# Performance work log

Measured on AMD Instinct MI355X. Metric: run time of the kernel, lower is better.

Reference implementation:

```python
import jax, jax.numpy as jnp
import numpy as np

T, D_MODEL, D_FF, N_EXPERTS, TOPK = 4096, 2048, 8192, 8, 2


def setup_inputs() -> dict:
    key = jax.random.key(0)
    k1, k2, k3, k4 = jax.random.split(key, 4)
    x = jax.random.normal(k1, (T, D_MODEL), dtype=jnp.float32)
    gating_output = jax.random.normal(k2, (T, N_EXPERTS), dtype=jnp.float32)
    # gate_proj and up_proj concatenated along output dim: [E, 2*d_ff, d_model]
    gate_up_proj = jax.random.normal(k3, (N_EXPERTS, 2 * D_FF, D_MODEL), dtype=jnp.float32) * 0.02
    # down_proj: [E, d_model, d_ff]
    down_proj = jax.random.normal(k4, (N_EXPERTS, D_MODEL, D_FF), dtype=jnp.float32) * 0.02
    return {"x": x, "gating_output": gating_output, "gate_up_proj": gate_up_proj,
            "down_proj": down_proj, "topk": TOPK}


def reference(x, gating_output, gate_up_proj, down_proj, topk):
    n_experts = gate_up_proj.shape[0]
    d_ff = down_proj.shape[2]
    # Router: fp32 softmax over experts, top-k, renormalize over the k selected.
    probs = jax.nn.softmax(gating_output.astype(jnp.float32), axis=1)  # [T, E]
    routing_weights, selected_experts = jax.lax.top_k(probs, topk)     # [T, k]
    routing_weights = routing_weights / jnp.sum(routing_weights, axis=-1, keepdims=True)
    routing_weights = routing_weights.astype(x.dtype)
    # Expert MLPs: silu(x @ Wg^T) * (x @ Wu^T) @ Wd^T, combined by routing weight.
    out = jnp.zeros_like(x)
    for e in range(n_experts):  # small fixed expert count
        coef = jnp.sum(jnp.where(selected_experts == e, routing_weights, 0.0), axis=-1)  # [T]
        gu = x @ gate_up_proj[e].T                     # [T, 2*d_ff]
        h = jax.nn.silu(gu[:, :d_ff]) * gu[:, d_ff:]   # [T, d_ff]
        out = out + coef[:, None] * (h @ down_proj[e].T)  # [T, d_model]
    return out
```

## Files before the change

kernel.cpp:

```cpp
#include <hip/hip_runtime.h>
#include <hip/hip_bf16.h>
#include <cstdint>
#include <cstddef>

#define T_TOK 4096
#define DMODEL 2048
#define DFF 8192
#define NEXP 8
#define NPAIR (T_TOK * 2)

typedef __bf16 bf16_t;
typedef __bf16 bf16x8 __attribute__((ext_vector_type(8)));
typedef float fx4 __attribute__((ext_vector_type(4)));

__global__ void router_kernel(const float* __restrict__ gating, int* __restrict__ counts,
                              int* __restrict__ tok_list, float* __restrict__ w_list) {
    int t = blockIdx.x * blockDim.x + threadIdx.x;
    if (t >= T_TOK) return;
    float l[NEXP];
    float mx = -1e30f;
#pragma unroll
    for (int e = 0; e < NEXP; e++) { l[e] = gating[t * NEXP + e]; mx = fmaxf(mx, l[e]); }
#pragma unroll
    for (int e = 0; e < NEXP; e++) { l[e] = __expf(l[e] - mx); }
    int e0 = 0; float p0 = l[0];
#pragma unroll
    for (int e = 1; e < NEXP; e++) { if (l[e] > p0) { p0 = l[e]; e0 = e; } }
    int e1 = -1; float p1 = -1.0f;
#pragma unroll
    for (int e = 0; e < NEXP; e++) { if (e != e0 && l[e] > p1) { p1 = l[e]; e1 = e; } }
    float inv = 1.0f / (p0 + p1);
    float w0 = p0 * inv, w1 = p1 * inv;
    int s0 = atomicAdd(&counts[e0], 1);
    tok_list[e0 * T_TOK + s0] = t; w_list[e0 * T_TOK + s0] = w0;
    int s1 = atomicAdd(&counts[e1], 1);
    tok_list[e1 * T_TOK + s1] = t; w_list[e1 * T_TOK + s1] = w1;
}

__global__ void scan_kernel(const int* __restrict__ counts, int* __restrict__ offsets) {
    if (threadIdx.x == 0 && blockIdx.x == 0) {
        int acc = 0;
        for (int e = 0; e < NEXP; e++) { offsets[e] = acc; acc += counts[e]; }
        offsets[NEXP] = acc;
    }
}

__global__ void cvt_x_kernel(const float* __restrict__ x, bf16_t* __restrict__ xb) {
    int i = blockIdx.x * blockDim.x + threadIdx.x;
    const fx4* src = (const fx4*)x;
    fx4 v0 = src[2 * i], v1 = src[2 * i + 1];
    bf16x8 o;
    o[0] = (bf16_t)v0[0]; o[1] = (bf16_t)v0[1]; o[2] = (bf16_t)v0[2]; o[3] = (bf16_t)v0[3];
    o[4] = (bf16_t)v1[0]; o[5] = (bf16_t)v1[1]; o[6] = (bf16_t)v1[2]; o[7] = (bf16_t)v1[3];
    *(bf16x8*)(xb + (size_t)i * 8) = o;
}

#define BM 128
#define BN 128
#define BK 64

__global__ __launch_bounds__(256, 2) void gateup_kernel(
    const bf16_t* __restrict__ xb, const float* __restrict__ gup,
    const int* __restrict__ counts, const int* __restrict__ offsets,
    const int* __restrict__ tok_list, bf16_t* __restrict__ h_buf)
{
    const int e = blockIdx.z;
    const int cnt = counts[e];
    const int mbase = blockIdx.y * BM;
    if (mbase >= cnt) return;
    const int nbase = blockIdx.x * BN;
    const int off_e = offsets[e];

    __shared__ bf16_t lds_a[BM * BK];
    __shared__ bf16_t lds_g[BN * BK];
    __shared__ bf16_t lds_u[BN * BK];

    const int tid = threadIdx.x;
    const int lane = tid & 63;
    const int w = tid >> 6;
    const int wm = (w >> 1) * 64, wn = (w & 1) * 64;

    const bf16_t* a_src[4];
    const float* g_src[4];
    const float* u_src[4];
    int st_lds[4];
    const float* gbase = gup + (size_t)e * (2 * DFF) * DMODEL;
#pragma unroll
    for (int t = 0; t < 4; t++) {
        int cid = t * 256 + tid;
        int row = cid >> 3, c = cid & 7;
        int slot = mbase + row;
        int tok = (slot < cnt) ? tok_list[e * T_TOK + slot] : 0;
        a_src[t] = xb + (size_t)tok * DMODEL + c * 8;
        g_src[t] = gbase + (size_t)(nbase + row) * DMODEL + c * 8;
        u_src[t] = gbase + (size_t)(DFF + nbase + row) * DMODEL + c * 8;
        st_lds[t] = row * BK + ((c ^ (row & 7)) * 8);
    }

    fx4 accg[4][4] = {};
    fx4 accu[4][4] = {};

    for (int k0 = 0; k0 < DMODEL; k0 += BK) {
#pragma unroll
        for (int t = 0; t < 4; t++) {
            *(uint4*)(&lds_a[st_lds[t]]) = *(const uint4*)(a_src[t] + k0);
            fx4 v0 = *(const fx4*)(g_src[t] + k0);
            fx4 v1 = *(const fx4*)(g_src[t] + k0 + 4);
            bf16x8 bg;
            bg[0] = (bf16_t)v0[0]; bg[1] = (bf16_t)v0[1]; bg[2] = (bf16_t)v0[2]; bg[3] = (bf16_t)v0[3];
            bg[4] = (bf16_t)v1[0]; bg[5] = (bf16_t)v1[1]; bg[6] = (bf16_t)v1[2]; bg[7] = (bf16_t)v1[3];
            *(bf16x8*)(&lds_g[st_lds[t]]) = bg;
            fx4 q0 = *(const fx4*)(u_src[t] + k0);
            fx4 q1 = *(const fx4*)(u_src[t] + k0 + 4);
            bf16x8 bu;
            bu[0] = (bf16_t)q0[0]; bu[1] = (bf16_t)q0[1]; bu[2] = (bf16_t)q0[2]; bu[3] = (bf16_t)q0[3];
            bu[4] = (bf16_t)q1[0]; bu[5] = (bf16_t)q1[1]; bu[6] = (bf16_t)q1[2]; bu[7] = (bf16_t)q1[3];
            *(bf16x8*)(&lds_u[st_lds[t]]) = bu;
        }
        __syncthreads();
#pragma unroll
        for (int kp = 0; kp < 2; kp++) {
            bf16x8 af[4], bfr[4];
            const int ke = kp * 4 + (lane >> 4);
#pragma unroll
            for (int m = 0; m < 4; m++) {
                int row = wm + m * 16 + (lane & 15);
                af[m] = *(const bf16x8*)(&lds_a[row * BK + ((ke ^ (row & 7)) * 8)]);
            }
#pragma unroll
            for (int n = 0; n < 4; n++) {
                int row = wn + n * 16 + (lane & 15);
                bfr[n] = *(const bf16x8*)(&lds_g[row * BK + ((ke ^ (row & 7)) * 8)]);
            }
#pragma unroll
            for (int m = 0; m < 4; m++)
#pragma unroll
                for (int n = 0; n < 4; n++)
                    accg[m][n] = __builtin_amdgcn_mfma_f32_16x16x32_bf16(af[m], bfr[n], accg[m][n], 0, 0, 0);
#pragma unroll
            for (int n = 0; n < 4; n++) {
                int row = wn + n * 16 + (lane & 15);
                bfr[n] = *(const bf16x8*)(&lds_u[row * BK + ((ke ^ (row & 7)) * 8)]);
            }
#pragma unroll
            for (int m = 0; m < 4; m++)
#pragma unroll
                for (int n = 0; n < 4; n++)
                    accu[m][n] = __builtin_amdgcn_mfma_f32_16x16x32_bf16(af[m], bfr[n], accu[m][n], 0, 0, 0);
        }
        __syncthreads();
    }

    const int colbase = nbase + wn + (lane & 15);
#pragma unroll
    for (int m = 0; m < 4; m++) {
        int rbase = wm + m * 16 + ((lane >> 4) * 4);
#pragma unroll
        for (int j = 0; j < 4; j++) {
            int slot = mbase + rbase + j;
            if (slot < cnt) {
                size_t hrow = (size_t)(off_e + slot);
#pragma unroll
                for (int n = 0; n < 4; n++) {
                    float g = accg[m][n][j];
                    float u = accu[m][n][j];
                    float hv = g * u / (1.0f + __expf(-g));
                    h_buf[hrow * DFF + colbase + n * 16] = (bf16_t)hv;
                }
            }
        }
    }
}

__global__ __launch_bounds__(256, 2) void down_kernel(
    const bf16_t* __restrict__ h_buf, const float* __restrict__ dwn,
    const int* __restrict__ counts, const int* __restrict__ offsets,
    const int* __restrict__ tok_list, const float* __restrict__ w_list,
    float* __restrict__ out)
{
    const int e = blockIdx.z;
    const int cnt = counts[e];
    const int mbase = blockIdx.y * BM;
    if (mbase >= cnt) return;
    const int nbase = blockIdx.x * BN;
    const int off_e = offsets[e];

    __shared__ bf16_t lds_a[BM * BK];
    __shared__ bf16_t lds_b[BN * BK];

    const int tid = threadIdx.x;
    const int lane = tid & 63;
    const int w = tid >> 6;
    const int wm = (w >> 1) * 64, wn = (w & 1) * 64;

    const bf16_t* a_src[4];
    const float* b_src[4];
    int st_lds[4];
    const float* bbase = dwn + (size_t)e * DMODEL * DFF;
#pragma unroll
    for (int t = 0; t < 4; t++) {
        int cid = t * 256 + tid;
        int row = cid >> 3, c = cid & 7;
        int hrow = off_e + mbase + row;
        if (hrow > NPAIR - 1) hrow = NPAIR - 1;
        a_src[t] = h_buf + (size_t)hrow * DFF + c * 8;
        b_src[t] = bbase + (size_t)(nbase + row) * DFF + c * 8;
        st_lds[t] = row * BK + ((c ^ (row & 7)) * 8);
    }

    fx4 acc[4][4] = {};

    for (int k0 = 0; k0 < DFF; k0 += BK) {
#pragma unroll
        for (int t = 0; t < 4; t++) {
            *(uint4*)(&lds_a[st_lds[t]]) = *(const uint4*)(a_src[t] + k0);
            fx4 v0 = *(const fx4*)(b_src[t] + k0);
            fx4 v1 = *(const fx4*)(b_src[t] + k0 + 4);
            bf16x8 bb;
            bb[0] = (bf16_t)v0[0]; bb[1] = (bf16_t)v0[1]; bb[2] = (bf16_t)v0[2]; bb[3] = (bf16_t)v0[3];
            bb[4] = (bf16_t)v1[0]; bb[5] = (bf16_t)v1[1]; bb[6] = (bf16_t)v1[2]; bb[7] = (bf16_t)v1[3];
            *(bf16x8*)(&lds_b[st_lds[t]]) = bb;
        }
        __syncthreads();
#pragma unroll
        for (int kp = 0; kp < 2; kp++) {
            bf16x8 af[4], bfr[4];
            const int ke = kp * 4 + (lane >> 4);
#pragma unroll
            for (int m = 0; m < 4; m++) {
                int row = wm + m * 16 + (lane & 15);
                af[m] = *(const bf16x8*)(&lds_a[row * BK + ((ke ^ (row & 7)) * 8)]);
            }
#pragma unroll
            for (int n = 0; n < 4; n++) {
                int row = wn + n * 16 + (lane & 15);
                bfr[n] = *(const bf16x8*)(&lds_b[row * BK + ((ke ^ (row & 7)) * 8)]);
            }
#pragma unroll
            for (int m = 0; m < 4; m++)
#pragma unroll
                for (int n = 0; n < 4; n++)
                    acc[m][n] = __builtin_amdgcn_mfma_f32_16x16x32_bf16(af[m], bfr[n], acc[m][n], 0, 0, 0);
        }
        __syncthreads();
    }

    const int colbase = nbase + wn + (lane & 15);
#pragma unroll
    for (int m = 0; m < 4; m++) {
        int rbase = wm + m * 16 + ((lane >> 4) * 4);
#pragma unroll
        for (int j = 0; j < 4; j++) {
            int slot = mbase + rbase + j;
            if (slot < cnt) {
                int tok = tok_list[e * T_TOK + slot];
                float wgt = w_list[e * T_TOK + slot];
#pragma unroll
                for (int n = 0; n < 4; n++) {
                    atomicAdd(&out[(size_t)tok * DMODEL + colbase + n * 16], wgt * acc[m][n][j]);
                }
            }
        }
    }
}

extern "C" void kernel_launch(void* const* d_in, const int* in_sizes, int n_in,
                              void* d_out, int out_size, void* d_ws, size_t ws_size,
                              hipStream_t stream) {
    const float* x      = (const float*)d_in[0];
    const float* gating = (const float*)d_in[1];
    const float* gup    = (const float*)d_in[2];
    const float* dwn    = (const float*)d_in[3];
    float* out = (float*)d_out;

    char* ws = (char*)d_ws;
    int*    counts   = (int*)(ws + 0);
    int*    offsets  = (int*)(ws + 64);
    int*    tok_list = (int*)(ws + 128);
    float*  w_list   = (float*)(ws + 128 + 131072);
    bf16_t* xb       = (bf16_t*)(ws + 262400);
    bf16_t* h_buf    = (bf16_t*)(ws + 17039872);

    hipMemsetAsync(counts, 0, 64, stream);
    hipMemsetAsync(out, 0, (size_t)out_size * sizeof(float), stream);

    router_kernel<<<dim3(T_TOK / 256), dim3(256), 0, stream>>>(gating, counts, tok_list, w_list);
    scan_kernel<<<dim3(1), dim3(64), 0, stream>>>(counts, offsets);
    cvt_x_kernel<<<dim3(T_TOK * DMODEL / 8 / 256), dim3(256), 0, stream>>>(x, xb);

    gateup_kernel<<<dim3(DFF / BN, T_TOK / BM, NEXP), dim3(256), 0, stream>>>(
        xb, gup, counts, offsets, tok_list, h_buf);

    down_kernel<<<dim3(DMODEL / BN, T_TOK / BM, NEXP), dim3(256), 0, stream>>>(
        h_buf, dwn, counts, offsets, tok_list, w_list, out);
}
```

Measured before the change: 1.614 ms.

## Narrow gate/up tiles, use direct global-to-LDS loads, and swizzle block order

The gate/up kernel now uses 64-column output tiles, with gate and up weights sharing one LDS buffer. This cuts LDS use and accumulator registers so three blocks fit per CU. Activation tiles in both GEMMs are loaded with global_load_lds, which writes straight into LDS and skips the round trip through registers. Block indices are remapped so consecutive blocks walk groups of 8 M tiles per N column, aiming for better L2 reuse of the weights. The trade-off is that each x tile is now reloaded for twice as many N tiles, and the weights are still converted from fp32 in the inner loop.

```diff
diff --git a/kernel.cpp b/kernel.cpp
--- a/kernel.cpp
+++ b/kernel.cpp
@@ -12,6 +12,19 @@
 typedef __bf16 bf16_t;
 typedef __bf16 bf16x8 __attribute__((ext_vector_type(8)));
 typedef float fx4 __attribute__((ext_vector_type(4)));
+
+__device__ __forceinline__ void gload16(const bf16_t* src, bf16_t* dst) {
+    __builtin_amdgcn_global_load_lds(
+        (const __attribute__((address_space(1))) uint32_t*)(src),
+        (__attribute__((address_space(3))) uint32_t*)(dst), 16, 0, 0);
+}
+
+__device__ __forceinline__ bf16x8 pack8(const fx4 lo, const fx4 hi) {
+    bf16x8 o;
+    o[0] = (bf16_t)lo[0]; o[1] = (bf16_t)lo[1]; o[2] = (bf16_t)lo[2]; o[3] = (bf16_t)lo[3];
+    o[4] = (bf16_t)hi[0]; o[5] = (bf16_t)hi[1]; o[6] = (bf16_t)hi[2]; o[7] = (bf16_t)hi[3];
+    return o;
+}
 
 __global__ void router_kernel(const float* __restrict__ gating, int* __restrict__ counts,
                               int* __restrict__ tok_list, float* __restrict__ w_list) {
@@ -30,11 +43,10 @@
 #pragma unroll
     for (int e = 0; e < NEXP; e++) { if (e != e0 && l[e] > p1) { p1 = l[e]; e1 = e; } }
     float inv = 1.0f / (p0 + p1);
-    float w0 = p0 * inv, w1 = p1 * inv;
     int s0 = atomicAdd(&counts[e0], 1);
-    tok_list[e0 * T_TOK + s0] = t; w_list[e0 * T_TOK + s0] = w0;
+    tok_list[e0 * T_TOK + s0] = t; w_list[e0 * T_TOK + s0] = p0 * inv;
     int s1 = atomicAdd(&counts[e1], 1);
-    tok_list[e1 * T_TOK + s1] = t; w_list[e1 * T_TOK + s1] = w1;
+    tok_list[e1 * T_TOK + s1] = t; w_list[e1 * T_TOK + s1] = p1 * inv;
 }
 
 __global__ void scan_kernel(const int* __restrict__ counts, int* __restrict__ offsets) {
@@ -49,121 +61,109 @@
     int i = blockIdx.x * blockDim.x + threadIdx.x;
     const fx4* src = (const fx4*)x;
     fx4 v0 = src[2 * i], v1 = src[2 * i + 1];
-    bf16x8 o;
-    o[0] = (bf16_t)v0[0]; o[1] = (bf16_t)v0[1]; o[2] = (bf16_t)v0[2]; o[3] = (bf16_t)v0[3];
-    o[4] = (bf16_t)v1[0]; o[5] = (bf16_t)v1[1]; o[6] = (bf16_t)v1[2]; o[7] = (bf16_t)v1[3];
-    *(bf16x8*)(xb + (size_t)i * 8) = o;
-}
-
-#define BM 128
-#define BN 128
-#define BK 64
-
-__global__ __launch_bounds__(256, 2) void gateup_kernel(
+    *(bf16x8*)(xb + (size_t)i * 8) = pack8(v0, v1);
+}
+
+__global__ __launch_bounds__(256, 3) void gateup_kernel(
     const bf16_t* __restrict__ xb, const float* __restrict__ gup,
     const int* __restrict__ counts, const int* __restrict__ offsets,
     const int* __restrict__ tok_list, bf16_t* __restrict__ h_buf)
 {
-    const int e = blockIdx.z;
+    const int e = blockIdx.y;
     const int cnt = counts[e];
-    const int mbase = blockIdx.y * BM;
+    const int s = blockIdx.x;
+    const int mbase = ((s >> 3) & 31) * 128;
     if (mbase >= cnt) return;
-    const int nbase = blockIdx.x * BN;
+    const int y = (s & 7) + 8 * (s >> 8);
+    const int nbase = y * 64;
     const int off_e = offsets[e];
 
-    __shared__ bf16_t lds_a[BM * BK];
-    __shared__ bf16_t lds_g[BN * BK];
-    __shared__ bf16_t lds_u[BN * BK];
+    __shared__ __align__(16) bf16_t lds_a[128 * 64];
+    __shared__ __align__(16) bf16_t lds_w[128 * 64];
 
     const int tid = threadIdx.x;
     const int lane = tid & 63;
     const int w = tid >> 6;
-    const int wm = (w >> 1) * 64, wn = (w & 1) * 64;
+    const int wm = (w >> 1) * 64;
+    const int wn = (w & 1) * 32;
 
     const bf16_t* a_src[4];
-    const float* g_src[4];
-    const float* u_src[4];
-    int st_lds[4];
+    bf16_t* a_dst[4];
+#pragma unroll
+    for (int j = 0; j < 4; j++) {
+        int sidx = (w * 4 + j) * 64 + lane;
+        int row = sidx >> 3;
+        int cc = (lane & 7) ^ (row & 7);
+        int slot = mbase + row;
+        int tok = (slot < cnt) ? tok_list[e * T_TOK + slot] : 0;
+        a_src[j] = xb + (size_t)tok * DMODEL + cc * 8;
+        a_dst[j] = lds_a + (w * 4 + j) * 512;
+    }
+    const float* w_src[4];
+    int w_st[4];
     const float* gbase = gup + (size_t)e * (2 * DFF) * DMODEL;
 #pragma unroll
     for (int t = 0; t < 4; t++) {
         int cid = t * 256 + tid;
         int row = cid >> 3, c = cid & 7;
-        int slot = mbase + row;
-        int tok = (slot < cnt) ? tok_list[e * T_TOK + slot] : 0;
-        a_src[t] = xb + (size_t)tok * DMODEL + c * 8;
-        g_src[t] = gbase + (size_t)(nbase + row) * DMODEL + c * 8;
-        u_src[t] = gbase + (size_t)(DFF + nbase + row) * DMODEL + c * 8;
-        st_lds[t] = row * BK + ((c ^ (row & 7)) * 8);
-    }
-
-    fx4 accg[4][4] = {};
-    fx4 accu[4][4] = {};
-
-    for (int k0 = 0; k0 < DMODEL; k0 += BK) {
+        int grow = (row < 64) ? (nbase + row) : (DFF + nbase + (row - 64));
+        w_src[t] = gbase + (size_t)grow * DMODEL + c * 8;
+        w_st[t] = row * 64 + ((c ^ (row & 7)) * 8);
+    }
+
+    fx4 accg[4][2] = {};
+    fx4 accu[4][2] = {};
+
+    for (int k0 = 0; k0 < DMODEL; k0 += 64) {
+#pragma unroll
+        for (int j = 0; j < 4; j++) { gload16(a_src[j], a_dst[j]); a_src[j] += 64; }
 #pragma unroll
         for (int t = 0; t < 4; t++) {
-            *(uint4*)(&lds_a[st_lds[t]]) = *(const uint4*)(a_src[t] + k0);
-            fx4 v0 = *(const fx4*)(g_src[t] + k0);
-            fx4 v1 = *(const fx4*)(g_src[t] + k0 + 4);
-            bf16x8 bg;
-            bg[0] = (bf16_t)v0[0]; bg[1] = (bf16_t)v0[1]; bg[2] = (bf16_t)v0[2]; bg[3] = (bf16_t)v0[3];
-            bg[4] = (bf16_t)v1[0]; bg[5] = (bf16_t)v1[1]; bg[6] = (bf16_t)v1[2]; bg[7] = (bf16_t)v1[3];
-            *(bf16x8*)(&lds_g[st_lds[t]]) = bg;
-            fx4 q0 = *(const fx4*)(u_src[t] + k0);
-            fx4 q1 = *(const fx4*)(u_src[t] + k0 + 4);
-            bf16x8 bu;
-            bu[0] = (bf16_t)q0[0]; bu[1] = (bf16_t)q0[1]; bu[2] = (bf16_t)q0[2]; bu[3] = (bf16_t)q0[3];
-            bu[4] = (bf16_t)q1[0]; bu[5] = (bf16_t)q1[1]; bu[6] = (bf16_t)q1[2]; bu[7] = (bf16_t)q1[3];
-            *(bf16x8*)(&lds_u[st_lds[t]]) = bu;
+            fx4 lo = *(const fx4*)(w_src[t]);
+            fx4 hi = *(const fx4*)(w_src[t] + 4);
+            w_src[t] += 64;
+            *(bf16x8*)(&lds_w[w_st[t]]) = pack8(lo, hi);
         }
         __syncthreads();
 #pragma unroll
         for (int kp = 0; kp < 2; kp++) {
-            bf16x8 af[4], bfr[4];
             const int ke = kp * 4 + (lane >> 4);
-#pragma unroll
-            for (int m = 0; m < 4; m++) {
-                int row = wm + m * 16 + (lane & 15);
-                af[m] = *(const bf16x8*)(&lds_a[row * BK + ((ke ^ (row & 7)) * 8)]);
-            }
-#pragma unroll
-            for (int n = 0; n < 4; n++) {
+            bf16x8 af[4], gf[2], uf[2];
+#pragma unroll
+            for (int i = 0; i < 4; i++) {
+                int row = wm + i * 16 + (lane & 15);
+                af[i] = *(const bf16x8*)(&lds_a[row * 64 + ((ke ^ (row & 7)) * 8)]);
+            }
+#pragma unroll
+            for (int n = 0; n < 2; n++) {
                 int row = wn + n * 16 + (lane & 15);
-                bfr[n] = *(const bf16x8*)(&lds_g[row * BK + ((ke ^ (row & 7)) * 8)]);
-            }
-#pragma unroll
-            for (int m = 0; m < 4; m++)
-#pragma unroll
-                for (int n = 0; n < 4; n++)
-                    accg[m][n] = __builtin_amdgcn_mfma_f32_16x16x32_bf16(af[m], bfr[n], accg[m][n], 0, 0, 0);
-#pragma unroll
-            for (int n = 0; n < 4; n++) {
-                int row = wn + n * 16 + (lane & 15);
-                bfr[n] = *(const bf16x8*)(&lds_u[row * BK + ((ke ^ (row & 7)) * 8)]);
-            }
-#pragma unroll
-            for (int m = 0; m < 4; m++)
-#pragma unroll
-                for (int n = 0; n < 4; n++)
-                    accu[m][n] = __builtin_amdgcn_mfma_f32_16x16x32_bf16(af[m], bfr[n], accu[m][n], 0, 0, 0);
+                gf[n] = *(const bf16x8*)(&lds_w[row * 64 + ((ke ^ (row & 7)) * 8)]);
+                uf[n] = *(const bf16x8*)(&lds_w[(row + 64) * 64 + ((ke ^ (row & 7)) * 8)]);
+            }
+#pragma unroll
+            for (int i = 0; i < 4; i++)
+#pragma unroll
+                for (int n = 0; n < 2; n++) {
+                    accg[i][n] = __builtin_amdgcn_mfma_f32_16x16x32_bf16(af[i], gf[n], accg[i][n], 0, 0, 0);
+                    accu[i][n] = __builtin_amdgcn_mfma_f32_16x16x32_bf16(af[i], uf[n], accu[i][n], 0, 0, 0);
+                }
         }
         __syncthreads();
     }
 
     const int colbase = nbase + wn + (lane & 15);
 #pragma unroll
-    for (int m = 0; m < 4; m++) {
-        int rbase = wm + m * 16 + ((lane >> 4) * 4);
+    for (int i = 0; i < 4; i++) {
+        int rbase = wm + i * 16 + ((lane >> 4) * 4);
 #pragma unroll
         for (int j = 0; j < 4; j++) {
             int slot = mbase + rbase + j;
             if (slot < cnt) {
                 size_t hrow = (size_t)(off_e + slot);
 #pragma unroll
-                for (int n = 0; n < 4; n++) {
-                    float g = accg[m][n][j];
-                    float u = accu[m][n][j];
+                for (int n = 0; n < 2; n++) {
+                    float g = accg[i][n][j];
+                    float u = accu[i][n][j];
                     float hv = g * u / (1.0f + __expf(-g));
                     h_buf[hrow * DFF + colbase + n * 16] = (bf16_t)hv;
                 }
@@ -172,83 +172,93 @@
     }
 }
 
-__global__ __launch_bounds__(256, 2) void down_kernel(
+__global__ __launch_bounds__(256, 3) void down_kernel(
     const bf16_t* __restrict__ h_buf, const float* __restrict__ dwn,
     const int* __restrict__ counts, const int* __restrict__ offsets,
     const int* __restrict__ tok_list, const float* __restrict__ w_list,
     float* __restrict__ out)
 {
-    const int e = blockIdx.z;
+    const int e = blockIdx.y;
     const int cnt = counts[e];
-    const int mbase = blockIdx.y * BM;
+    const int s = blockIdx.x;
+    const int mbase = ((s >> 3) & 31) * 128;
     if (mbase >= cnt) return;
-    const int nbase = blockIdx.x * BN;
+    const int y = (s & 7) + 8 * (s >> 8);
+    const int nbase = y * 128;
     const int off_e = offsets[e];
 
-    __shared__ bf16_t lds_a[BM * BK];
-    __shared__ bf16_t lds_b[BN * BK];
+    __shared__ __align__(16) bf16_t lds_a[128 * 64];
+    __shared__ __align__(16) bf16_t lds_b[128 * 64];
 
     const int tid = threadIdx.x;
     const int lane = tid & 63;
     const int w = tid >> 6;
-    const int wm = (w >> 1) * 64, wn = (w & 1) * 64;
+    const int wm = (w >> 1) * 64;
+    const int wn = (w & 1) * 64;
 
     const bf16_t* a_src[4];
+    bf16_t* a_dst[4];
+#pragma unroll
+    for (int j = 0; j < 4; j++) {
+        int sidx = (w * 4 + j) * 64 + lane;
+        int row = sidx >> 3;
+        int cc = (lane & 7) ^ (row & 7);
+        int hrow = off_e + mbase + row;
+        if (hrow > NPAIR - 1) hrow = NPAIR - 1;
+        a_src[j] = h_buf + (size_t)hrow * DFF + cc * 8;
+        a_dst[j] = lds_a + (w * 4 + j) * 512;
+    }
     const float* b_src[4];
-    int st_lds[4];
+    int b_st[4];
     const float* bbase = dwn + (size_t)e * DMODEL * DFF;
 #pragma unroll
     for (int t = 0; t < 4; t++) {
         int cid = t * 256 + tid;
         int row = cid >> 3, c = cid & 7;
-        int hrow = off_e + mbase + row;
-        if (hrow > NPAIR - 1) hrow = NPAIR - 1;
-        a_src[t] = h_buf + (size_t)hrow * DFF + c * 8;
         b_src[t] = bbase + (size_t)(nbase + row) * DFF + c * 8;
-        st_lds[t] = row * BK + ((c ^ (row & 7)) * 8);
+        b_st[t] = row * 64 + ((c ^ (row & 7)) * 8);
     }
 
     fx4 acc[4][4] = {};
 
-    for (int k0 = 0; k0 < DFF; k0 += BK) {
+    for (int k0 = 0; k0 < DFF; k0 += 64) {
+#pragma unroll
+        for (int j = 0; j < 4; j++) { gload16(a_src[j], a_dst[j]); a_src[j] += 64; }
 #pragma unroll
         for (int t = 0; t < 4; t++) {
-            *(uint4*)(&lds_a[st_lds[t]]) = *(const uint4*)(a_src[t] + k0);
-            fx4 v0 = *(const fx4*)(b_src[t] + k0);
-            fx4 v1 = *(const fx4*)(b_src[t] + k0 + 4);
-            bf16x8 bb;
-            bb[0] = (bf16_t)v0[0]; bb[1] = (bf16_t)v0[1]; bb[2] = (bf16_t)v0[2]; bb[3] = (bf16_t)v0[3];
-            bb[4] = (bf16_t)v1[0]; bb[5] = (bf16_t)v1[1]; bb[6] = (bf16_t)v1[2]; bb[7] = (bf16_t)v1[3];
-            *(bf16x8*)(&lds_b[st_lds[t]]) = bb;
+            fx4 lo = *(const fx4*)(b_src[t]);
+            fx4 hi = *(const fx4*)(b_src[t] + 4);
+            b_src[t] += 64;
+            *(bf16x8*)(&lds_b[b_st[t]]) = pack8(lo, hi);
         }
         __syncthreads();
 #pragma unroll
         for (int kp = 0; kp < 2; kp++) {
+            const int ke = kp * 4 + (lane >> 4);
             bf16x8 af[4], bfr[4];
-            const int ke = kp * 4 + (lane >> 4);
-#pragma unroll
-            for (int m = 0; m < 4; m++) {
-                int row = wm + m * 16 + (lane & 15);
-                af[m] = *(const bf16x8*)(&lds_a[row * BK + ((ke ^ (row & 7)) * 8)]);
+#pragma unroll
+            for (int i = 0; i < 4; i++) {
+                int row = wm + i * 16 + (lane & 15);
+                af[i] = *(const bf16x8*)(&lds_a[row * 64 + ((ke ^ (row & 7)) * 8)]);
             }
 #pragma unroll
             for (int n = 0; n < 4; n++) {
                 int row = wn + n * 16 + (lane & 15);
-                bfr[n] = *(const bf16x8*)(&lds_b[row * BK + ((ke ^ (row & 7)) * 8)]);
-            }
-#pragma unroll
-            for (int m = 0; m < 4; m++)
+                bfr[n] = *(const bf16x8*)(&lds_b[row * 64 + ((ke ^ (row & 7)) * 8)]);
+            }
+#pragma unroll
+            for (int i = 0; i < 4; i++)
 #pragma unroll
                 for (int n = 0; n < 4; n++)
-                    acc[m][n] = __builtin_amdgcn_mfma_f32_16x16x32_bf16(af[m], bfr[n], acc[m][n], 0, 0, 0);
+                    acc[i][n] = __builtin_amdgcn_mfma_f32_16x16x32_bf16(af[i], bfr[n], acc[i][n], 0, 0, 0);
         }
         __syncthreads();
     }
 
     const int colbase = nbase + wn + (lane & 15);
 #pragma unroll
-    for (int m = 0; m < 4; m++) {
-        int rbase = wm + m * 16 + ((lane >> 4) * 4);
+    for (int i = 0; i < 4; i++) {
+        int rbase = wm + i * 16 + ((lane >> 4) * 4);
 #pragma unroll
         for (int j = 0; j < 4; j++) {
             int slot = mbase + rbase + j;
@@ -256,9 +266,8 @@
                 int tok = tok_list[e * T_TOK + slot];
                 float wgt = w_list[e * T_TOK + slot];
 #pragma unroll
-                for (int n = 0; n < 4; n++) {
-                    atomicAdd(&out[(size_t)tok * DMODEL + colbase + n * 16], wgt * acc[m][n][j]);
-                }
+                for (int n = 0; n < 4; n++)
+                    atomicAdd(&out[(size_t)tok * DMODEL + colbase + n * 16], wgt * acc[i][n][j]);
             }
         }
     }
@@ -288,9 +297,9 @@
     scan_kernel<<<dim3(1), dim3(64), 0, stream>>>(counts, offsets);
     cvt_x_kernel<<<dim3(T_TOK * DMODEL / 8 / 256), dim3(256), 0, stream>>>(x, xb);
 
-    gateup_kernel<<<dim3(DFF / BN, T_TOK / BM, NEXP), dim3(256), 0, stream>>>(
+    gateup_kernel<<<dim3(4096, NEXP), dim3(256), 0, stream>>>(
         xb, gup, counts, offsets, tok_list, h_buf);
 
-    down_kernel<<<dim3(DMODEL / BN, T_TOK / BM, NEXP), dim3(256), 0, stream>>>(
+    down_kernel<<<dim3(512, NEXP), dim3(256), 0, stream>>>(
         h_buf, dwn, counts, offsets, tok_list, w_list, out);
 }
```

Result: no change. 1.599 ms (-0.9%).
